# Optimization experiments

Hardware: AMD Instinct MI355X
Metric: run time of the kernel (lower is better)

The kernel has to match this reference:

```python
import jax, jax.numpy as jnp
import numpy as np

NUM_BANDS = 8
NUM_CHANNELS = 16
KC = NUM_BANDS * NUM_CHANNELS
EMA_KERNEL_LENGTH = 100
DELTA = 0.1
EPS = 1e-06
S_INIT = 0.04


def setup_inputs() -> dict:
    key = jax.random.key(0)
    kx, = jax.random.split(key, 1)
    x = jax.random.normal(kx, (32, NUM_BANDS, NUM_CHANNELS, 8192), dtype=jnp.float32)
    alpha_raw = jnp.zeros((KC,), dtype=jnp.float32)
    log_s = jnp.full((KC,), float(np.log(S_INIT / (1.0 - S_INIT))), dtype=jnp.float32)
    return {"x": x, "alpha_raw": alpha_raw, "log_s": log_s}


def _build_ema_kernel(log_s):
    # (KC, 1, L_full) causal EMA kernel, then caller slices last L taps
    Lf = EMA_KERNEL_LENGTH
    s = jax.nn.sigmoid(log_s)                      # (KC,)
    j = jnp.arange(Lf, dtype=s.dtype)              # (Lf,)
    impulse = s[:, None] * (1.0 - s[:, None]) ** j[None, :]   # (KC, Lf)
    impulse = impulse / (impulse.sum(axis=1, keepdims=True) + 1e-08)
    kernel = impulse[:, ::-1]                      # flip to causal conv kernel
    return kernel[:, None, :]                      # (KC, 1, Lf)


def reference(x, alpha_raw, log_s):
    B, K, C, T = x.shape
    x_flat = x.reshape(B, KC, T)
    alpha = jax.nn.sigmoid(alpha_raw) * 0.5        # (KC,) in (0, 0.5)
    x_mag = jnp.abs(x_flat)
    L = min(EMA_KERNEL_LENGTH, T)
    kernel = _build_ema_kernel(log_s)[:, :, -L:]   # (KC, 1, L)
    x_padded = jnp.pad(x_mag, ((0, 0), (0, 0), (L - 1, 0)))
    # depthwise causal conv: groups = KC
    M = jax.lax.conv_general_dilated(
        x_padded, kernel,
        window_strides=(1,), padding='VALID',
        feature_group_count=KC,
        dimension_numbers=('NCH', 'OIH', 'NCH'))   # (B, KC, T)
    gain = jnp.clip(M, EPS, None) ** alpha[None, :, None] + DELTA
    out_flat = x_flat / gain
    return out_flat.reshape(B, K, C, T)
```

## Files before the change

kernel.cpp:

```cpp
#include <hip/hip_runtime.h>
#include <math.h>


constexpr int T      = 8192;
constexpr int KC_    = 128;
constexpr int LEN    = 100;
constexpr int BLOCK  = 256;
constexpr int CHUNK  = 32;
constexpr float EPS_   = 1e-6f;
constexpr float DELTA_ = 0.1f;
constexpr float LOG2E  = 1.4426950408889634f;

__device__ __forceinline__ int skew(int t) { return t + (t >> 5); }

__device__ __forceinline__ float fast_sigmoid(float x) {
    const float e = __builtin_amdgcn_exp2f(-x * LOG2E);
    return __builtin_amdgcn_rcpf(1.0f + e);
}

__global__ __launch_bounds__(BLOCK, 4) void agc_kernel(
    const float* __restrict__ x,
    const float* __restrict__ alpha_raw,
    const float* __restrict__ log_s,
    float* __restrict__ out)
{
    __shared__ float lx[T + (T >> 5)];

    const int row = blockIdx.x;
    const int kc  = row & (KC_ - 1);
    const int tid = threadIdx.x;
    const float* __restrict__ xrow = x + (size_t)row * T;
    float* __restrict__ orow       = out + (size_t)row * T;

    #pragma unroll
    for (int it = 0; it < (T / 4) / BLOCK; ++it) {
        const int i = tid + it * BLOCK;
        const float4 v = reinterpret_cast<const float4*>(xrow)[i];
        const int a = skew(i * 4);
        lx[a]     = v.x;
        lx[a + 1] = v.y;
        lx[a + 2] = v.z;
        lx[a + 3] = v.w;
    }

    const float s     = fast_sigmoid(log_s[kc]);
    const float alpha = 0.5f * fast_sigmoid(alpha_raw[kc]);
    const float q     = 1.0f - s;
    const float q100  = __builtin_amdgcn_exp2f(100.0f * __builtin_amdgcn_logf(q));
    const float norm  = (1.0f - q100) + 1e-8f;
    const float w0    = s / norm;
    const float c3    = w0 * q100;

    __syncthreads();

    const int t0 = tid * CHUNK;
    float M;
    {
        const float q2 = q * q;
        const float q3 = q2 * q;
        const float q4 = q2 * q2;
        const int jmax  = (t0 >= LEN - 1) ? LEN : (t0 + 1);
        const int jmax4 = jmax & ~3;
        float m0 = 0.0f, m1 = 0.0f, m2 = 0.0f, m3 = 0.0f;
        float wj = w0;
        int j = 0;
        for (; j < jmax4; j += 4) {
            m0 = fmaf(wj,      fabsf(lx[skew(t0 - j)]),     m0);
            m1 = fmaf(wj * q,  fabsf(lx[skew(t0 - j - 1)]), m1);
            m2 = fmaf(wj * q2, fabsf(lx[skew(t0 - j - 2)]), m2);
            m3 = fmaf(wj * q3, fabsf(lx[skew(t0 - j - 3)]), m3);
            wj *= q4;
        }
        for (; j < jmax; ++j) {
            m0 = fmaf(wj, fabsf(lx[skew(t0 - j)]), m0);
            wj *= q;
        }
        M = (m0 + m1) + (m2 + m3);
    }

    float xv = lx[skew(t0)];
    #pragma unroll
    for (int k4 = 0; k4 < CHUNK / 4; ++k4) {
        float4 o;
        float* op = &o.x;
        #pragma unroll
        for (int u = 0; u < 4; ++u) {
            const int k = k4 * 4 + u;
            const int t = t0 + k;
            if (k > 0) {
                xv = lx[skew(t)];
                const int tb = t - LEN;
                const float xb = (tb >= 0) ? fabsf(lx[skew(tb)]) : 0.0f;
                M = q * M + w0 * fabsf(xv) - c3 * xb;
            }
            const float Mc = fmaxf(M, EPS_);
            const float g  = __builtin_amdgcn_exp2f(alpha * __builtin_amdgcn_logf(Mc)) + DELTA_;
            op[u] = xv * __builtin_amdgcn_rcpf(g);
        }
        reinterpret_cast<float4*>(orow)[(t0 >> 2) + k4] = o;
    }
}

extern "C" void kernel_launch(void* const* d_in, const int* in_sizes, int n_in,
                              void* d_out, int out_size, void* d_ws, size_t ws_size,
                              hipStream_t stream) {
    const float* x         = (const float*)d_in[0];
    const float* alpha_raw = (const float*)d_in[1];
    const float* log_s     = (const float*)d_in[2];
    float* out             = (float*)d_out;
    const int nrows = in_sizes[0] / T;
    agc_kernel<<<nrows, BLOCK, 0, stream>>>(x, alpha_raw, log_s, out);
}
```

Before: 266.8 us.

## Stage row in LDS as fp16 with paired loads and higher occupancy

Input rows are now stored in shared memory as half precision, so LDS use per block is halved and launch bounds go from 4 to 8 blocks per CU. The EMA warm-up and recurrence read pairs of values with half2 loads, using a specialised fully unrolled path for chunks away from the row start. Output x is also read back from fp16, which loses precision in both the gain estimate and the numerator and may exceed tolerance. The kernel is memory-bound, so the gain from extra occupancy may be limited.

```diff
diff --git a/kernel.cpp b/kernel.cpp
--- a/kernel.cpp
+++ b/kernel.cpp
@@ -1,4 +1,5 @@
 #include <hip/hip_runtime.h>
+#include <hip/hip_fp16.h>
 #include <math.h>
 
 
@@ -11,20 +12,26 @@
 constexpr float DELTA_ = 0.1f;
 constexpr float LOG2E  = 1.4426950408889634f;
 
-__device__ __forceinline__ int skew(int t) { return t + (t >> 5); }
+__device__ __forceinline__ int sk(int t) { return t + ((t >> 5) << 1); }
 
 __device__ __forceinline__ float fast_sigmoid(float x) {
     const float e = __builtin_amdgcn_exp2f(-x * LOG2E);
     return __builtin_amdgcn_rcpf(1.0f + e);
 }
 
-__global__ __launch_bounds__(BLOCK, 4) void agc_kernel(
+__device__ __forceinline__ float gain_div(float xv, float M, float alpha) {
+    const float Mc = fmaxf(M, EPS_);
+    const float g  = __builtin_amdgcn_exp2f(alpha * __builtin_amdgcn_logf(Mc)) + DELTA_;
+    return xv * __builtin_amdgcn_rcpf(g);
+}
+
+__global__ __launch_bounds__(BLOCK, 8) void agc_kernel(
     const float* __restrict__ x,
     const float* __restrict__ alpha_raw,
     const float* __restrict__ log_s,
     float* __restrict__ out)
 {
-    __shared__ float lx[T + (T >> 5)];
+    __shared__ __half lh[T + ((T >> 5) << 1)];
 
     const int row = blockIdx.x;
     const int kc  = row & (KC_ - 1);
@@ -36,11 +43,9 @@
     for (int it = 0; it < (T / 4) / BLOCK; ++it) {
         const int i = tid + it * BLOCK;
         const float4 v = reinterpret_cast<const float4*>(xrow)[i];
-        const int a = skew(i * 4);
-        lx[a]     = v.x;
-        lx[a + 1] = v.y;
-        lx[a + 2] = v.z;
-        lx[a + 3] = v.w;
+        const int e = sk(i * 4);
+        *reinterpret_cast<__half2*>(&lh[e])     = __float22half2_rn(make_float2(v.x, v.y));
+        *reinterpret_cast<__half2*>(&lh[e + 2]) = __float22half2_rn(make_float2(v.z, v.w));
     }
 
     const float s     = fast_sigmoid(log_s[kc]);
@@ -54,50 +59,65 @@
     __syncthreads();
 
     const int t0 = tid * CHUNK;
-    float M;
-    {
-        const float q2 = q * q;
-        const float q3 = q2 * q;
-        const float q4 = q2 * q2;
-        const int jmax  = (t0 >= LEN - 1) ? LEN : (t0 + 1);
-        const int jmax4 = jmax & ~3;
-        float m0 = 0.0f, m1 = 0.0f, m2 = 0.0f, m3 = 0.0f;
+
+    auto ld2 = [&](int t) -> float2 {
+        return __half22float2(*reinterpret_cast<const __half2*>(&lh[sk(t)]));
+    };
+
+    if (t0 >= 128) {
+        float m0 = 0.0f, m1 = 0.0f;
+        const float qq = q * q;
+        float whi = w0 * q;
+        float wlo = whi * q;
+        #pragma unroll 7
+        for (int i = 0; i < 49; ++i) {
+            const float2 f = ld2(t0 - 2 * i - 2);
+            m0 = fmaf(wlo, fabsf(f.x), m0);
+            m1 = fmaf(whi, fabsf(f.y), m1);
+            wlo *= qq; whi *= qq;
+        }
+        {
+            const float2 f = ld2(t0 - LEN);
+            m1 = fmaf(whi, fabsf(f.y), m1);
+        }
+        float M = m0 + m1;
+
+        float o[4];
+        #pragma unroll
+        for (int m = 0; m < CHUNK / 2; ++m) {
+            const float2 xf = ld2(t0 + 2 * m);
+            const float2 xb = ld2(t0 - LEN + 2 * m);
+            if (m == 0) M = fmaf(w0, fabsf(xf.x), M);
+            else        M = fmaf(q, M, fmaf(w0, fabsf(xf.x), -c3 * fabsf(xb.x)));
+            o[(2 * m)     & 3] = gain_div(xf.x, M, alpha);
+            M = fmaf(q, M, fmaf(w0, fabsf(xf.y), -c3 * fabsf(xb.y)));
+            o[(2 * m + 1) & 3] = gain_div(xf.y, M, alpha);
+            if (m & 1)
+                reinterpret_cast<float4*>(orow)[(t0 >> 2) + (m >> 1)] =
+                    make_float4(o[0], o[1], o[2], o[3]);
+        }
+    } else {
+        float M = 0.0f;
         float wj = w0;
-        int j = 0;
-        for (; j < jmax4; j += 4) {
-            m0 = fmaf(wj,      fabsf(lx[skew(t0 - j)]),     m0);
-            m1 = fmaf(wj * q,  fabsf(lx[skew(t0 - j - 1)]), m1);
-            m2 = fmaf(wj * q2, fabsf(lx[skew(t0 - j - 2)]), m2);
-            m3 = fmaf(wj * q3, fabsf(lx[skew(t0 - j - 3)]), m3);
-            wj *= q4;
-        }
-        for (; j < jmax; ++j) {
-            m0 = fmaf(wj, fabsf(lx[skew(t0 - j)]), m0);
+        for (int j = 0; j <= t0; ++j) {
+            M = fmaf(wj, fabsf((float)lh[sk(t0 - j)]), M);
             wj *= q;
         }
-        M = (m0 + m1) + (m2 + m3);
-    }
-
-    float xv = lx[skew(t0)];
-    #pragma unroll
-    for (int k4 = 0; k4 < CHUNK / 4; ++k4) {
-        float4 o;
-        float* op = &o.x;
+        float o[4];
         #pragma unroll
-        for (int u = 0; u < 4; ++u) {
-            const int k = k4 * 4 + u;
+        for (int k = 0; k < CHUNK; ++k) {
             const int t = t0 + k;
+            const float xv = (float)lh[sk(t)];
             if (k > 0) {
-                xv = lx[skew(t)];
                 const int tb = t - LEN;
-                const float xb = (tb >= 0) ? fabsf(lx[skew(tb)]) : 0.0f;
-                M = q * M + w0 * fabsf(xv) - c3 * xb;
+                const float xb = (tb >= 0) ? fabsf((float)lh[sk(tb)]) : 0.0f;
+                M = fmaf(q, M, fmaf(w0, fabsf(xv), -c3 * xb));
             }
-            const float Mc = fmaxf(M, EPS_);
-            const float g  = __builtin_amdgcn_exp2f(alpha * __builtin_amdgcn_logf(Mc)) + DELTA_;
-            op[u] = xv * __builtin_amdgcn_rcpf(g);
+            o[k & 3] = gain_div(xv, M, alpha);
+            if ((k & 3) == 3)
+                reinterpret_cast<float4*>(orow)[(t0 >> 2) + (k >> 2)] =
+                    make_float4(o[0], o[1], o[2], o[3]);
         }
-        reinterpret_cast<float4*>(orow)[(t0 >> 2) + k4] = o;
     }
 }
 
```

New measurement: 262.8 us. Within noise of the previous version (-1.5%).
